# Performance work log

Measured on AMD Instinct MI355X. Metric: run time of the kernel, lower is better.

## Reference

```python
import jax, jax.numpy as jnp
import numpy as np

DIM = 256
HEADS = 4
AG_HID = 512
MIN_TOK = 64  # topk fallback size from the torch code


def _ln(x, g, b):
    # LayerNorm over last dim, eps=1e-5 (torch default)
    m = x.mean(-1, keepdims=True)
    v = ((x - m) ** 2).mean(-1, keepdims=True)
    return (x - m) / jnp.sqrt(v + 1e-5) * g + b


def _mixer(x, sel, lng, lnb, wqkv, bqkv, wo, bo, w1, b1, w2, b2):
    # MixerBlock: pre-LN MHA + pre-LN FFN (same LN module used twice).
    # Attention restricted to selected tokens via key mask -> identical math to
    # gathering the selected subset and attending within it (LN/FFN are per-token;
    # outputs at non-selected positions are discarded by the caller).
    B, N, D = x.shape
    dh = D // HEADS
    xn = _ln(x, lng, lnb)
    qkv = xn @ wqkv.T + bqkv
    q, k, v = jnp.split(qkv, 3, axis=-1)
    q = q.reshape(B, N, HEADS, dh)
    k = k.reshape(B, N, HEADS, dh)
    v = v.reshape(B, N, HEADS, dh)
    s = jnp.einsum('bqhd,bkhd->bhqk', q, k) / np.float32(np.sqrt(dh))
    s = jnp.where(sel[:, None, None, :], s, jnp.float32(-1e9))
    a = jax.nn.softmax(s, axis=-1)
    o = jnp.einsum('bhqk,bkhd->bqhd', a, v).reshape(B, N, D) @ wo.T + bo
    x = x + o
    xn2 = _ln(x, lng, lnb)
    h = jax.nn.gelu(xn2 @ w1.T + b1, approximate=False)
    return x + h @ w2.T + b2


def _mixer_params(key, d, scale=0.02):
    ks = jax.random.split(key, 8)
    return dict(
        lng=jnp.ones((d,), jnp.float32),
        lnb=jnp.zeros((d,), jnp.float32),
        wqkv=jax.random.normal(ks[0], (3 * d, d), jnp.float32) * scale,
        bqkv=jnp.zeros((3 * d,), jnp.float32),
        wo=jax.random.normal(ks[1], (d, d), jnp.float32) * scale,
        bo=jnp.zeros((d,), jnp.float32),
        w1=jax.random.normal(ks[2], (4 * d, d), jnp.float32) * scale,
        b1=jnp.zeros((4 * d,), jnp.float32),
        w2=jax.random.normal(ks[3], (d, 4 * d), jnp.float32) * scale,
        b2=jnp.zeros((d,), jnp.float32),
    )


def setup_inputs() -> dict:
    key = jax.random.key(0)
    k = jax.random.split(key, 8)
    B, C, H, W = 4, DIM, 48, 48
    inp = {
        'f_ir': jax.random.normal(k[0], (B, C, H, W), jnp.float32),
        'f_vis': jax.random.normal(k[1], (B, C, H, W), jnp.float32),
        # SamplingAgent: two 1x1 convs (pure channel mixes)
        'aw1': jax.random.normal(k[2], (AG_HID, 2 * DIM), jnp.float32) * 0.02,
        'ab1': jnp.zeros((AG_HID,), jnp.float32),
        'aw2': jax.random.normal(k[3], (1, AG_HID), jnp.float32) * 0.02,
        'ab2': jnp.zeros((1,), jnp.float32),
    }
    for name, kk in (('ir', k[4]), ('vis', k[5])):
        for pn, pv in _mixer_params(kk, DIM).items():
            inp[f'{name}_{pn}'] = pv
    return inp


def reference(f_ir, f_vis, aw1, ab1, aw2, ab2,
              ir_lng, ir_lnb, ir_wqkv, ir_bqkv, ir_wo, ir_bo, ir_w1, ir_b1, ir_w2, ir_b2,
              vis_lng, vis_lnb, vis_wqkv, vis_bqkv, vis_wo, vis_bo, vis_w1, vis_b1, vis_w2, vis_b2):
    B, C, H, W = f_ir.shape
    N = H * W
    base = (f_ir + f_vis).reshape(B, C, N).transpose(0, 2, 1)  # [B,N,C]
    # SamplingAgent (1x1 convs == per-pixel channel MLP)
    x = jnp.concatenate([f_ir, f_vis], axis=1)
    h1 = jax.nn.silu(jnp.einsum('bchw,oc->bohw', x, aw1) + ab1[None, :, None, None])
    logits = jnp.einsum('bchw,oc->bohw', h1, aw2) + ab2[None, :, None, None]  # [B,1,H,W]
    lf = logits.reshape(B, N)
    mask = (lf > 0).astype(f_ir.dtype)                 # selection_mask_ste (inference)
    count = mask.sum(axis=1)
    # fallback: top-64 agent logits if fewer than 64 selected
    _, idx = jax.lax.top_k(lf, MIN_TOK)
    topm = jnp.zeros((B, N), bool).at[jnp.arange(B)[:, None], idx].set(True)
    sel = jnp.where((count < MIN_TOK)[:, None], topm, mask > 0.5)  # effective selected set
    ti = f_ir.reshape(B, C, N).transpose(0, 2, 1)
    tv = f_vis.reshape(B, C, N).transpose(0, 2, 1)
    ri = _mixer(ti, sel, ir_lng, ir_lnb, ir_wqkv, ir_bqkv, ir_wo, ir_bo, ir_w1, ir_b1, ir_w2, ir_b2)
    rv = _mixer(tv, sel, vis_lng, vis_lnb, vis_wqkv, vis_bqkv, vis_wo, vis_bo, vis_w1, vis_b1, vis_w2, vis_b2)
    refined = (ri + rv) * mask[:, :, None]             # m_ste multiplier at selected positions
    out = jnp.where(sel[:, :, None], refined, base)    # scatter-combine into canvas
    return out.transpose(0, 2, 1).reshape(B, C, H, W)
```

## Files before the change

### kernel.cpp

```cpp
#include <hip/hip_runtime.h>
#include <hip/hip_bf16.h>
#include <math.h>

#define NTOK 2304
#define CDIM 256
#define NH 4
#define DHD 64

typedef __hip_bfloat16 bf16;

__device__ __forceinline__ float blk_sum256(float v, float* red){
  int t = threadIdx.x;
  red[t] = v; __syncthreads();
  #pragma unroll
  for (int s = 128; s > 0; s >>= 1){
    if (t < s) red[t] += red[t+s];
    __syncthreads();
  }
  float r = red[0]; __syncthreads();
  return r;
}

__device__ __forceinline__ void fma4(const float4 w, const float* x, int c, float& acc){
  acc += w.x*x[c] + w.y*x[c+1] + w.z*x[c+2] + w.w*x[c+3];
}

__device__ __forceinline__ float bfu(unsigned short s){
  union{unsigned u; float f;} a; a.u = ((unsigned)s)<<16; return a.f;
}

__global__ __launch_bounds__(256) void k_fill(float* __restrict__ out, int n, float v){
  int i = blockIdx.x*256 + threadIdx.x;
  if (i < n) out[i] = v;
}

__global__ __launch_bounds__(256) void k_agent(const float* __restrict__ fir, const float* __restrict__ fvis,
    const float* __restrict__ aw1, const float* __restrict__ ab1,
    const float* __restrict__ aw2, const float* __restrict__ ab2,
    float* __restrict__ lf)
{
  __shared__ float xv[512];
  __shared__ float red[256];
  int t = threadIdx.x;
  int pix = blockIdx.x;
  int b = pix / NTOK, n = pix % NTOK;
  xv[t]     = fir [(size_t)(b*CDIM + t)*NTOK + n];
  xv[t+256] = fvis[(size_t)(b*CDIM + t)*NTOK + n];
  __syncthreads();
  float part = 0.f;
  #pragma unroll
  for (int oi = 0; oi < 2; ++oi){
    int o = t + oi*256;
    const float4* w4 = reinterpret_cast<const float4*>(aw1 + (size_t)o*512);
    float acc = ab1[o];
    #pragma unroll 8
    for (int c4 = 0; c4 < 128; ++c4){
      fma4(w4[c4], xv, c4*4, acc);
    }
    float s = acc / (1.f + expf(-acc));
    part += s * aw2[o];
  }
  float tot = blk_sum256(part, red);
  if (t == 0) lf[pix] = tot + ab2[0];
}

__global__ __launch_bounds__(256) void k_select(const float* __restrict__ lf,
    float* __restrict__ msk, int* __restrict__ sel)
{
  __shared__ float vals[NTOK];
  __shared__ int   ired[256];
  __shared__ float rmax[256];
  __shared__ int   rix[256];
  int b = blockIdx.x;
  int t = threadIdx.x;
  int cnt = 0;
  for (int n = t; n < NTOK; n += 256){
    float v = lf[b*NTOK + n];
    vals[n] = v;
    int m = (v > 0.f) ? 1 : 0;
    msk[b*NTOK + n] = (float)m;
    sel[b*NTOK + n] = m;
    cnt += m;
  }
  ired[t] = cnt; __syncthreads();
  #pragma unroll
  for (int s = 128; s > 0; s >>= 1){
    if (t < s) ired[t] += ired[t+s];
    __syncthreads();
  }
  int count = ired[0];
  __syncthreads();
  if (count < 64){
    for (int n = t; n < NTOK; n += 256) sel[b*NTOK + n] = 0;
    __syncthreads();
    for (int it = 0; it < 64; ++it){
      float bestv = -INFINITY; int besti = t;
      for (int n = t; n < NTOK; n += 256){
        float v = vals[n];
        if (v > bestv || (v == bestv && n < besti)){ bestv = v; besti = n; }
      }
      rmax[t] = bestv; rix[t] = besti; __syncthreads();
      #pragma unroll
      for (int s = 128; s > 0; s >>= 1){
        if (t < s){
          if (rmax[t+s] > rmax[t] || (rmax[t+s] == rmax[t] && rix[t+s] < rix[t])){
            rmax[t] = rmax[t+s]; rix[t] = rix[t+s];
          }
        }
        __syncthreads();
      }
      if (t == 0){
        int w = rix[0];
        if (w >= 0 && w < NTOK){ sel[b*NTOK + w] = 1; vals[w] = -INFINITY; }
      }
      __syncthreads();
    }
  }
}

__global__ __launch_bounds__(256) void k_ln_qkv(const float* __restrict__ f,
    const float* __restrict__ lng, const float* __restrict__ lnb,
    const float* __restrict__ wqkv, const float* __restrict__ bqkv,
    float* __restrict__ qkv)
{
  __shared__ float xn[256];
  __shared__ float red[256];
  int t = threadIdx.x;
  int pix = blockIdx.x;
  int b = pix / NTOK, n = pix % NTOK;
  float x = f[(size_t)(b*CDIM + t)*NTOK + n];
  float m  = blk_sum256(x,   red) * (1.f/256.f);
  float sq = blk_sum256(x*x, red) * (1.f/256.f);
  float rstd = rsqrtf(sq - m*m + 1e-5f);
  xn[t] = (x - m)*rstd*lng[t] + lnb[t];
  __syncthreads();
  size_t obase = (size_t)pix * 768;
  #pragma unroll
  for (int oi = 0; oi < 3; ++oi){
    int o = t + oi*256;
    const float4* w4 = reinterpret_cast<const float4*>(wqkv + (size_t)o*256);
    float acc = bqkv[o];
    #pragma unroll 8
    for (int c4 = 0; c4 < 64; ++c4){
      fma4(w4[c4], xn, c4*4, acc);
    }
    qkv[obase + o] = acc;
  }
}

__global__ __launch_bounds__(256) void k_attn(const float* __restrict__ qkv,
    const int* __restrict__ sel, float* __restrict__ attno)
{
  __shared__ float Qs[64*68];
  __shared__ float Ks[64*68];
  __shared__ float Vs[64*68];
  __shared__ float Ps[64*68];
  __shared__ int selk[64];
  int tid = threadIdx.x;
  int w  = tid >> 6;
  int l  = tid & 63;
  int kg = l & 15;
  int qh = l >> 4;
  int qbase = w*16 + qh;
  int bi = blockIdx.x;
  int qt = bi % 36; int h = (bi/36) % NH; int b = bi / (36*NH);

  for (int c = tid; c < 1024; c += 256){
    int r = c >> 4, d4 = c & 15;
    float4 v = *(const float4*)(qkv + (size_t)(b*NTOK + qt*64 + r)*768 + h*64 + d4*4);
    *(float4*)(Qs + r*68 + d4*4) = v;
  }

  float m_[4], l_[4], o_[4][4];
  #pragma unroll
  for (int i = 0; i < 4; ++i){
    m_[i] = -INFINITY; l_[i] = 0.f;
    o_[i][0]=0.f; o_[i][1]=0.f; o_[i][2]=0.f; o_[i][3]=0.f;
  }

  for (int kt = 0; kt < 36; ++kt){
    __syncthreads();
    for (int c = tid; c < 1024; c += 256){
      int r = c >> 4, d4 = c & 15;
      size_t base = (size_t)(b*NTOK + kt*64 + r)*768 + h*64 + d4*4;
      *(float4*)(Ks + r*68 + d4*4) = *(const float4*)(qkv + base + 256);
      *(float4*)(Vs + r*68 + d4*4) = *(const float4*)(qkv + base + 512);
    }
    if (tid < 64) selk[tid] = sel[b*NTOK + kt*64 + tid];
    __syncthreads();

    float s[4][4];
    #pragma unroll
    for (int i = 0; i < 4; ++i){ s[i][0]=0.f; s[i][1]=0.f; s[i][2]=0.f; s[i][3]=0.f; }
    #pragma unroll 4
    for (int d4 = 0; d4 < 16; ++d4){
      float4 qv[4], kv[4];
      #pragma unroll
      for (int i = 0; i < 4; ++i) qv[i] = *(const float4*)(Qs + (qbase+4*i)*68 + d4*4);
      #pragma unroll
      for (int j = 0; j < 4; ++j) kv[j] = *(const float4*)(Ks + (kg+16*j)*68 + d4*4);
      #pragma unroll
      for (int i = 0; i < 4; ++i){
        #pragma unroll
        for (int j = 0; j < 4; ++j){
          s[i][j] += qv[i].x*kv[j].x + qv[i].y*kv[j].y + qv[i].z*kv[j].z + qv[i].w*kv[j].w;
        }
      }
    }
    int ms0 = selk[kg], ms1 = selk[kg+16], ms2 = selk[kg+32], ms3 = selk[kg+48];
    #pragma unroll
    for (int i = 0; i < 4; ++i){
      s[i][0] = ms0 ? s[i][0]*0.125f : -1e9f;
      s[i][1] = ms1 ? s[i][1]*0.125f : -1e9f;
      s[i][2] = ms2 ? s[i][2]*0.125f : -1e9f;
      s[i][3] = ms3 ? s[i][3]*0.125f : -1e9f;
    }
    float p[4][4];
    #pragma unroll
    for (int i = 0; i < 4; ++i){
      float mx = fmaxf(fmaxf(s[i][0], s[i][1]), fmaxf(s[i][2], s[i][3]));
      #pragma unroll
      for (int off = 8; off; off >>= 1) mx = fmaxf(mx, __shfl_xor(mx, off, 16));
      float mnew = fmaxf(m_[i], mx);
      float fs = expf(m_[i] - mnew);
      p[i][0] = expf(s[i][0] - mnew); p[i][1] = expf(s[i][1] - mnew);
      p[i][2] = expf(s[i][2] - mnew); p[i][3] = expf(s[i][3] - mnew);
      float ps = p[i][0] + p[i][1] + p[i][2] + p[i][3];
      #pragma unroll
      for (int off = 8; off; off >>= 1) ps += __shfl_xor(ps, off, 16);
      l_[i] = l_[i]*fs + ps; m_[i] = mnew;
      o_[i][0]*=fs; o_[i][1]*=fs; o_[i][2]*=fs; o_[i][3]*=fs;
    }
    #pragma unroll
    for (int i = 0; i < 4; ++i){
      Ps[(qbase+4*i)*68 + kg     ] = p[i][0];
      Ps[(qbase+4*i)*68 + kg + 16] = p[i][1];
      Ps[(qbase+4*i)*68 + kg + 32] = p[i][2];
      Ps[(qbase+4*i)*68 + kg + 48] = p[i][3];
    }
    #pragma unroll 4
    for (int k4 = 0; k4 < 16; ++k4){
      float4 pv[4], vv[4];
      #pragma unroll
      for (int i = 0; i < 4; ++i) pv[i] = *(const float4*)(Ps + (qbase+4*i)*68 + k4*4);
      #pragma unroll
      for (int jj = 0; jj < 4; ++jj) vv[jj] = *(const float4*)(Vs + (k4*4+jj)*68 + kg*4);
      #pragma unroll
      for (int i = 0; i < 4; ++i){
        o_[i][0] += pv[i].x*vv[0].x + pv[i].y*vv[1].x + pv[i].z*vv[2].x + pv[i].w*vv[3].x;
        o_[i][1] += pv[i].x*vv[0].y + pv[i].y*vv[1].y + pv[i].z*vv[2].y + pv[i].w*vv[3].y;
        o_[i][2] += pv[i].x*vv[0].z + pv[i].y*vv[1].z + pv[i].z*vv[2].z + pv[i].w*vv[3].z;
        o_[i][3] += pv[i].x*vv[0].w + pv[i].y*vv[1].w + pv[i].z*vv[2].w + pv[i].w*vv[3].w;
      }
    }
  }
  #pragma unroll
  for (int i = 0; i < 4; ++i){
    float inv = 1.f / l_[i];
    int row = qt*64 + qbase + 4*i;
    float4 ov; ov.x = o_[i][0]*inv; ov.y = o_[i][1]*inv; ov.z = o_[i][2]*inv; ov.w = o_[i][3]*inv;
    *(float4*)(attno + (size_t)(b*NTOK + row)*256 + h*64 + kg*4) = ov;
  }
}

__global__ __launch_bounds__(256) void k_oproj_ln(const float* __restrict__ attno,
    const float* __restrict__ wo, const float* __restrict__ bo,
    const float* __restrict__ f,
    const float* __restrict__ lng, const float* __restrict__ lnb,
    float* __restrict__ x1, float* __restrict__ xn_out)
{
  __shared__ float orow[256];
  __shared__ float red[256];
  int t = threadIdx.x;
  int pix = blockIdx.x;
  int b = pix / NTOK, n = pix % NTOK;
  orow[t] = attno[(size_t)pix*256 + t];
  __syncthreads();
  const float4* w4 = reinterpret_cast<const float4*>(wo + (size_t)t*256);
  float acc = bo[t];
  #pragma unroll 8
  for (int c4 = 0; c4 < 64; ++c4){
    fma4(w4[c4], orow, c4*4, acc);
  }
  float v = acc + f[(size_t)(b*CDIM + t)*NTOK + n];
  x1[(size_t)pix*256 + t] = v;
  float m  = blk_sum256(v,   red) * (1.f/256.f);
  float sq = blk_sum256(v*v, red) * (1.f/256.f);
  float rstd = rsqrtf(sq - m*m + 1e-5f);
  xn_out[(size_t)pix*256 + t] = (v - m)*rstd*lng[t] + lnb[t];
}

__global__ __launch_bounds__(256) void k_gemm1(const float* __restrict__ xn,
    const float* __restrict__ w1, const float* __restrict__ b1,
    bf16* __restrict__ H)
{
  __shared__ float Xs[64*68];
  __shared__ float Ws[64*68];
  int tid = threadIdx.x;
  int bp = blockIdx.x % 144, bh = blockIdx.x / 144;
  int pi = tid & 15, hj = tid >> 4;
  float acc[4][4] = {{0.f}};
  for (int k0 = 0; k0 < 256; k0 += 64){
    __syncthreads();
    for (int c = tid; c < 1024; c += 256){
      int r = c >> 4, f4 = c & 15;
      *(float4*)(Xs + r*68 + f4*4) = *(const float4*)(xn + (size_t)(bp*64 + r)*256 + k0 + f4*4);
      *(float4*)(Ws + r*68 + f4*4) = *(const float4*)(w1 + (size_t)(bh*64 + r)*256 + k0 + f4*4);
    }
    __syncthreads();
    #pragma unroll 4
    for (int k4 = 0; k4 < 16; ++k4){
      float4 xv[4], wv[4];
      #pragma unroll
      for (int i = 0; i < 4; ++i) xv[i] = *(const float4*)(Xs + (pi+16*i)*68 + k4*4);
      #pragma unroll
      for (int j = 0; j < 4; ++j) wv[j] = *(const float4*)(Ws + (hj+16*j)*68 + k4*4);
      #pragma unroll
      for (int i = 0; i < 4; ++i){
        #pragma unroll
        for (int j = 0; j < 4; ++j){
          acc[i][j] += xv[i].x*wv[j].x + xv[i].y*wv[j].y + xv[i].z*wv[j].z + xv[i].w*wv[j].w;
        }
      }
    }
  }
  #pragma unroll
  for (int i = 0; i < 4; ++i){
    int p = bp*64 + pi + 16*i;
    #pragma unroll
    for (int j = 0; j < 4; ++j){
      int hh = bh*64 + hj + 16*j;
      float v = acc[i][j] + b1[hh];
      v = 0.5f*v*(1.f + erff(v*0.70710678118654752f));
      H[(size_t)p*1024 + hh] = __float2bfloat16(v);
    }
  }
}

__global__ __launch_bounds__(256) void k_gemm2(const bf16* __restrict__ H,
    const float* __restrict__ w2, const float* __restrict__ b2,
    const float* __restrict__ x1, float* __restrict__ mo, int accum)
{
  __shared__ float Hs[64*68];
  __shared__ float Ws[64*68];
  int tid = threadIdx.x;
  int bp = blockIdx.x % 144, bo = blockIdx.x / 144;
  int pi = tid & 15, oj = tid >> 4;
  float acc[4][4] = {{0.f}};
  for (int k0 = 0; k0 < 1024; k0 += 64){
    __syncthreads();
    for (int c = tid; c < 1024; c += 256){
      int r = c >> 4, f4 = c & 15;
      const ushort4 u = *(const ushort4*)(H + (size_t)(bp*64 + r)*1024 + k0 + f4*4);
      float4 hv; hv.x = bfu(u.x); hv.y = bfu(u.y); hv.z = bfu(u.z); hv.w = bfu(u.w);
      *(float4*)(Hs + r*68 + f4*4) = hv;
      *(float4*)(Ws + r*68 + f4*4) = *(const float4*)(w2 + (size_t)(bo*64 + r)*1024 + k0 + f4*4);
    }
    __syncthreads();
    #pragma unroll 4
    for (int k4 = 0; k4 < 16; ++k4){
      float4 hv[4], wv[4];
      #pragma unroll
      for (int i = 0; i < 4; ++i) hv[i] = *(const float4*)(Hs + (pi+16*i)*68 + k4*4);
      #pragma unroll
      for (int j = 0; j < 4; ++j) wv[j] = *(const float4*)(Ws + (oj+16*j)*68 + k4*4);
      #pragma unroll
      for (int i = 0; i < 4; ++i){
        #pragma unroll
        for (int j = 0; j < 4; ++j){
          acc[i][j] += hv[i].x*wv[j].x + hv[i].y*wv[j].y + hv[i].z*wv[j].z + hv[i].w*wv[j].w;
        }
      }
    }
  }
  #pragma unroll
  for (int i = 0; i < 4; ++i){
    int p = bp*64 + pi + 16*i;
    #pragma unroll
    for (int j = 0; j < 4; ++j){
      int o = bo*64 + oj + 16*j;
      size_t idx = (size_t)p*256 + o;
      float v = acc[i][j] + b2[o] + x1[idx];
      mo[idx] = accum ? (mo[idx] + v) : v;
    }
  }
}

__global__ __launch_bounds__(256) void k_combine(const float* __restrict__ fir, const float* __restrict__ fvis,
    const int* __restrict__ sel, const float* __restrict__ msk,
    const float* __restrict__ mo, float* __restrict__ out)
{
  size_t i = (size_t)blockIdx.x*256 + threadIdx.x;
  int n = (int)(i % NTOK);
  size_t bc = i / NTOK;
  int cc = (int)(bc % CDIM);
  int b  = (int)(bc / CDIM);
  float base = fir[i] + fvis[i];
  int bn = b*NTOK + n;
  float r;
  if (sel[bn]){
    r = mo[(size_t)bn*256 + cc] * msk[bn];
  } else {
    r = base;
  }
  out[i] = r;
}

extern "C" void kernel_launch(void* const* d_in, const int* in_sizes, int n_in,
                              void* d_out, int out_size, void* d_ws, size_t ws_size,
                              hipStream_t stream)
{
  static const int expected[26] = {
    2359296, 2359296, 262144, 512, 512, 1,
    256, 256, 196608, 768, 65536, 256, 262144, 1024, 262144, 256,
    256, 256, 196608, 768, 65536, 256, 262144, 1024, 262144, 256
  };
  const size_t WS_NEEDED = 37859328;
  float sentinel = 0.f; bool fail = false;
  if (n_in != 26){ sentinel = 1e9f; fail = true; }
  else {
    for (int i = 0; i < 26; ++i){
      if (in_sizes[i] != expected[i]){ sentinel = 1e6f * (float)(i+1); fail = true; break; }
    }
    if (!fail && ws_size < WS_NEEDED){ sentinel = 100.f + (float)(ws_size >> 10); fail = true; }
  }
  if (fail){
    k_fill<<<(out_size + 255)/256, 256, 0, stream>>>((float*)d_out, out_size, sentinel);
    return;
  }

  const float* fir  = (const float*)d_in[0];
  const float* fvis = (const float*)d_in[1];
  const float* aw1  = (const float*)d_in[2];
  const float* ab1  = (const float*)d_in[3];
  const float* aw2  = (const float*)d_in[4];
  const float* ab2  = (const float*)d_in[5];

  char* wsb = (char*)d_ws;
  float* lf    = (float*)(wsb + 0);
  float* msk   = (float*)(wsb + 36864);
  int*   sel   = (int*)  (wsb + 73728);
  float* mo    = (float*)(wsb + 110592);
  float* qkv   = (float*)(wsb + 9547776);
  float* x1    = (float*)(wsb + 9547776);
  bf16*  H     = (bf16*) (wsb + 9547776 + 9437184);
  float* attno = (float*)d_out;
  float* xn    = (float*)d_out;

  k_agent<<<4*NTOK, 256, 0, stream>>>(fir, fvis, aw1, ab1, aw2, ab2, lf);
  k_select<<<4, 256, 0, stream>>>(lf, msk, sel);

  for (int mdl = 0; mdl < 2; ++mdl){
    const float* f = mdl ? fvis : fir;
    int p = 6 + mdl*10;
    const float* lng  = (const float*)d_in[p+0];
    const float* lnb  = (const float*)d_in[p+1];
    const float* wqkv = (const float*)d_in[p+2];
    const float* bqkv = (const float*)d_in[p+3];
    const float* wo   = (const float*)d_in[p+4];
    const float* bo   = (const float*)d_in[p+5];
    const float* w1   = (const float*)d_in[p+6];
    const float* b1   = (const float*)d_in[p+7];
    const float* w2   = (const float*)d_in[p+8];
    const float* b2   = (const float*)d_in[p+9];
    k_ln_qkv  <<<4*NTOK, 256, 0, stream>>>(f, lng, lnb, wqkv, bqkv, qkv);
    k_attn    <<<4*NH*(NTOK/64), 256, 0, stream>>>(qkv, sel, attno);
    k_oproj_ln<<<4*NTOK, 256, 0, stream>>>(attno, wo, bo, f, lng, lnb, x1, xn);
    k_gemm1   <<<144*16, 256, 0, stream>>>(xn, w1, b1, H);
    k_gemm2   <<<144*4, 256, 0, stream>>>(H, w2, b2, x1, mo, mdl);
  }

  k_combine<<<(4*CDIM*NTOK)/256, 256, 0, stream>>>(fir, fvis, sel, msk, mo, (float*)d_out);
}
```

Baseline: 5.201 ms.

## Replace per-pixel agent MLP with transposed-input tiled GEMM and atomic reduction

The sampling-agent 1x1 conv previously ran one block per pixel, each re-reading all 512x512 weights with strided channel loads. It now transposes the inputs into a token-major buffer and computes the first conv as a 64x64 register-tiled shared-memory GEMM. The SiLU and second conv are fused into the epilogue, and partial logits are accumulated with atomics, with the bias moved into the select kernel. This adds a transpose pass, a fill kernel and float atomics whose summation order is nondeterministic, which could flip near-zero logits.

```diff
diff --git a/kernel.cpp b/kernel.cpp
--- a/kernel.cpp
+++ b/kernel.cpp
@@ -34,37 +34,101 @@
   if (i < n) out[i] = v;
 }
 
-__global__ __launch_bounds__(256) void k_agent(const float* __restrict__ fir, const float* __restrict__ fvis,
+__global__ __launch_bounds__(256) void k_xt(const float* __restrict__ fir, const float* __restrict__ fvis,
+    float* __restrict__ XT)
+{
+  __shared__ float S[64*68];
+  int tid = threadIdx.x;
+  int bi = blockIdx.x;
+  int ct = bi & 7;
+  int nt = (bi >> 3) % 36;
+  int b  = bi / (36*8);
+  const float* src = (ct < 4) ? fir : fvis;
+  int c0 = (ct & 3) * 64;
+  for (int c = tid; c < 1024; c += 256){
+    int cr = c >> 4, n4 = c & 15;
+    *(float4*)(S + cr*68 + n4*4) =
+      *(const float4*)(src + (size_t)(b*CDIM + c0 + cr)*NTOK + nt*64 + n4*4);
+  }
+  __syncthreads();
+  for (int c = tid; c < 1024; c += 256){
+    int nr = c >> 4, c4 = c & 15;
+    float4 v;
+    v.x = S[(c4*4+0)*68 + nr];
+    v.y = S[(c4*4+1)*68 + nr];
+    v.z = S[(c4*4+2)*68 + nr];
+    v.w = S[(c4*4+3)*68 + nr];
+    *(float4*)(XT + (size_t)(b*NTOK + nt*64 + nr)*512 + ct*64 + c4*4) = v;
+  }
+}
+
+__global__ __launch_bounds__(256) void k_agent_g(const float* __restrict__ XT,
     const float* __restrict__ aw1, const float* __restrict__ ab1,
-    const float* __restrict__ aw2, const float* __restrict__ ab2,
-    float* __restrict__ lf)
-{
-  __shared__ float xv[512];
-  __shared__ float red[256];
-  int t = threadIdx.x;
-  int pix = blockIdx.x;
-  int b = pix / NTOK, n = pix % NTOK;
-  xv[t]     = fir [(size_t)(b*CDIM + t)*NTOK + n];
-  xv[t+256] = fvis[(size_t)(b*CDIM + t)*NTOK + n];
+    const float* __restrict__ aw2, float* __restrict__ lf)
+{
+  __shared__ float Xs[64*68];
+  __shared__ float Ws[64*68];
+  __shared__ float Rs[64*17];
+  int tid = threadIdx.x;
+  int bi = blockIdx.x;
+  int ot = bi & 7;
+  int nt = (bi >> 3) % 36;
+  int b  = bi / (36*8);
+  int pixbase = b*NTOK + nt*64;
+  int o0 = ot*64;
+  int pi = tid & 15, oj = tid >> 4;
+  float acc[4][4] = {{0.f}};
+  for (int k0 = 0; k0 < 512; k0 += 64){
+    __syncthreads();
+    for (int c = tid; c < 1024; c += 256){
+      int r = c >> 4, f4 = c & 15;
+      *(float4*)(Xs + r*68 + f4*4) = *(const float4*)(XT  + (size_t)(pixbase + r)*512 + k0 + f4*4);
+      *(float4*)(Ws + r*68 + f4*4) = *(const float4*)(aw1 + (size_t)(o0 + r)*512 + k0 + f4*4);
+    }
+    __syncthreads();
+    #pragma unroll 4
+    for (int k4 = 0; k4 < 16; ++k4){
+      float4 xv[4], wv[4];
+      #pragma unroll
+      for (int i = 0; i < 4; ++i) xv[i] = *(const float4*)(Xs + (pi+16*i)*68 + k4*4);
+      #pragma unroll
+      for (int j = 0; j < 4; ++j) wv[j] = *(const float4*)(Ws + (oj+16*j)*68 + k4*4);
+      #pragma unroll
+      for (int i = 0; i < 4; ++i){
+        #pragma unroll
+        for (int j = 0; j < 4; ++j){
+          acc[i][j] += xv[i].x*wv[j].x + xv[i].y*wv[j].y + xv[i].z*wv[j].z + xv[i].w*wv[j].w;
+        }
+      }
+    }
+  }
+  float part[4];
+  #pragma unroll
+  for (int i = 0; i < 4; ++i){
+    float p = 0.f;
+    #pragma unroll
+    for (int j = 0; j < 4; ++j){
+      int o = o0 + oj + 16*j;
+      float v = acc[i][j] + ab1[o];
+      float s = v / (1.f + expf(-v));
+      p += s * aw2[o];
+    }
+    part[i] = p;
+  }
   __syncthreads();
-  float part = 0.f;
-  #pragma unroll
-  for (int oi = 0; oi < 2; ++oi){
-    int o = t + oi*256;
-    const float4* w4 = reinterpret_cast<const float4*>(aw1 + (size_t)o*512);
-    float acc = ab1[o];
-    #pragma unroll 8
-    for (int c4 = 0; c4 < 128; ++c4){
-      fma4(w4[c4], xv, c4*4, acc);
-    }
-    float s = acc / (1.f + expf(-acc));
-    part += s * aw2[o];
-  }
-  float tot = blk_sum256(part, red);
-  if (t == 0) lf[pix] = tot + ab2[0];
+  #pragma unroll
+  for (int i = 0; i < 4; ++i) Rs[(pi + 16*i)*17 + oj] = part[i];
+  __syncthreads();
+  if (tid < 64){
+    float s = 0.f;
+    #pragma unroll
+    for (int j = 0; j < 16; ++j) s += Rs[tid*17 + j];
+    atomicAdd(lf + pixbase + tid, s);
+  }
 }
 
 __global__ __launch_bounds__(256) void k_select(const float* __restrict__ lf,
+    const float* __restrict__ ab2,
     float* __restrict__ msk, int* __restrict__ sel)
 {
   __shared__ float vals[NTOK];
@@ -73,9 +137,10 @@
   __shared__ int   rix[256];
   int b = blockIdx.x;
   int t = threadIdx.x;
+  float ab2f = ab2[0];
   int cnt = 0;
   for (int n = t; n < NTOK; n += 256){
-    float v = lf[b*NTOK + n];
+    float v = lf[b*NTOK + n] + ab2f;
     vals[n] = v;
     int m = (v > 0.f) ? 1 : 0;
     msk[b*NTOK + n] = (float)m;
@@ -441,14 +506,17 @@
   float* msk   = (float*)(wsb + 36864);
   int*   sel   = (int*)  (wsb + 73728);
   float* mo    = (float*)(wsb + 110592);
+  float* XT    = (float*)(wsb + 9547776);
   float* qkv   = (float*)(wsb + 9547776);
   float* x1    = (float*)(wsb + 9547776);
   bf16*  H     = (bf16*) (wsb + 9547776 + 9437184);
   float* attno = (float*)d_out;
   float* xn    = (float*)d_out;
 
-  k_agent<<<4*NTOK, 256, 0, stream>>>(fir, fvis, aw1, ab1, aw2, ab2, lf);
-  k_select<<<4, 256, 0, stream>>>(lf, msk, sel);
+  k_fill   <<<36, 256, 0, stream>>>(lf, 9216, 0.f);
+  k_xt     <<<1152, 256, 0, stream>>>(fir, fvis, XT);
+  k_agent_g<<<1152, 256, 0, stream>>>(XT, aw1, ab1, aw2, lf);
+  k_select <<<4, 256, 0, stream>>>(lf, ab2, msk, sel);
 
   for (int mdl = 0; mdl < 2; ++mdl){
     const float* f = mdl ? fvis : fir;
```

Result: faster. 4.289 ms (-17.5%).
